# Kernel tuning notes

Hardware: AMD Instinct MI355X
Metric: run time of the kernel (lower is better)

Reference implementation:

```python
import jax, jax.numpy as jnp
import numpy as np

B, S, HID, NH = 2, 2048, 2048, 16
HD = HID // NH  # 128
BASE = 10000.0


def rope_tables(seq_len, head_dim):
    inv_freq = 1.0 / (BASE ** (jnp.arange(0, head_dim, 2, dtype=jnp.float32) / head_dim))
    t = jnp.arange(seq_len, dtype=jnp.float32)
    freqs = jnp.einsum('i,j->ij', t, inv_freq)        # [s, d/2]
    emb = jnp.concatenate([freqs, freqs], axis=-1)     # [s, d]
    return jnp.cos(emb), jnp.sin(emb)


def apply_rotary(x, cos, sin):
    # x: [b, s, h, d]; cos/sin: [s, d]
    x1, x2 = x[..., ::2], x[..., 1::2]
    c = cos[None, :, None, ::2]
    s = sin[None, :, None, ::2]
    x1r = x1 * c - x2 * s
    x2r = x1 * s + x2 * c
    return jnp.stack([x1r, x2r], axis=-1).reshape(x.shape)


def setup_inputs() -> dict:
    key = jax.random.key(0)
    ks = jax.random.split(key, 5)
    scale = 1.0 / np.sqrt(HID)
    hidden_states = jax.random.normal(ks[0], (B, S, HID), jnp.float32)
    Wq = jax.random.normal(ks[1], (HID, HID), jnp.float32) * scale
    Wk = jax.random.normal(ks[2], (HID, HID), jnp.float32) * scale
    Wv = jax.random.normal(ks[3], (HID, HID), jnp.float32) * scale
    Wo = jax.random.normal(ks[4], (HID, HID), jnp.float32) * scale
    causal = jnp.tril(jnp.ones((S, S), dtype=bool))
    attention_mask = jnp.where(causal, 0.0, -1e9).astype(jnp.float32)[None, :, :]  # [1, S, S]
    return {'hidden_states': hidden_states, 'Wq': Wq, 'Wk': Wk, 'Wv': Wv,
            'Wo': Wo, 'attention_mask': attention_mask}


def reference(hidden_states, Wq, Wk, Wv, Wo, attention_mask):
    b, s, hid = hidden_states.shape
    q = (hidden_states @ Wq.T).reshape(b, s, NH, HD)
    k = (hidden_states @ Wk.T).reshape(b, s, NH, HD)
    v = (hidden_states @ Wv.T).reshape(b, s, NH, HD)
    cos, sin = rope_tables(s, HD)
    q = apply_rotary(q, cos, sin)
    k = apply_rotary(k, cos, sin)
    # [b, h, s, d]
    q = q.transpose(0, 2, 1, 3)
    k = k.transpose(0, 2, 1, 3)
    v = v.transpose(0, 2, 1, 3)
    scores = jnp.einsum('bhqd,bhkd->bhqk', q, k) / np.sqrt(HD).astype(np.float32)
    scores = scores + attention_mask[:, None, :, :]  # broadcast mask over heads
    probs = jax.nn.softmax(scores.astype(jnp.float32), axis=-1).astype(q.dtype)
    attn = jnp.einsum('bhqk,bhkd->bhqd', probs, v)
    attn = attn.transpose(0, 2, 1, 3).reshape(b, s, hid)
    return attn @ Wo.T
```

## Files before the change

### kernel.cpp

```cpp
#include <hip/hip_runtime.h>
#include <math.h>

typedef __attribute__((ext_vector_type(8))) short short8;
typedef __attribute__((ext_vector_type(4))) float f32x4;
typedef __attribute__((ext_vector_type(16))) float f32x16;
typedef __attribute__((ext_vector_type(4))) float fvec4;
typedef __attribute__((ext_vector_type(4))) unsigned short us4;
typedef __attribute__((ext_vector_type(2))) unsigned int uint2v;

#define DI __device__ __forceinline__
#define BARX asm volatile("s_barrier" ::: "memory")
#define WAITV6 asm volatile("s_waitcnt vmcnt(6)" ::: "memory")
#define WAITV0 asm volatile("s_waitcnt vmcnt(0)" ::: "memory")
#define WAITL0 asm volatile("s_waitcnt lgkmcnt(0)" ::: "memory")
#define SCHED0 __builtin_amdgcn_sched_barrier(0)

constexpr int BB = 2, SS = 2048, HIDc = 2048, NHc = 16, HDc = 128;
constexpr int MT = BB * SS;
constexpr int KC = HIDc;

constexpr size_t OFF_HB  = 0;
constexpr size_t OFF_WB  = OFF_HB + (size_t)MT * KC * 2;
constexpr size_t OFF_Q   = OFF_WB + (size_t)4 * HIDc * KC * 2;
constexpr size_t OFF_K   = OFF_Q  + (size_t)BB * NHc * SS * HDc * 2;
constexpr size_t OFF_V   = OFF_K  + (size_t)BB * NHc * SS * HDc * 2;
constexpr size_t OFF_ATT = OFF_V  + (size_t)BB * NHc * SS * HDc * 2;
constexpr size_t OFF_COS = OFF_ATT + (size_t)MT * HIDc * 2;
constexpr size_t OFF_SIN = OFF_COS + (size_t)SS * 32 * 4;
constexpr size_t WS_NEED = OFF_SIN + (size_t)SS * 32 * 4;

DI float bf2f(unsigned short u) { union { unsigned u; float f; } v; v.u = (unsigned)u << 16; return v.f; }
DI unsigned short f2bf(float f) {
  union { float f; unsigned u; } v; v.f = f;
  unsigned r = v.u + 0x7fffu + ((v.u >> 16) & 1u);
  return (unsigned short)(r >> 16);
}

DI void gload_lds16(const void* g, void* l) {
  __builtin_amdgcn_global_load_lds((const __attribute__((address_space(1))) void*)g,
                                   (__attribute__((address_space(3))) void*)l, 16, 0, 0);
}

DI unsigned cvtpk_bf16(float lo, float hi_) {
  unsigned r;
  asm("v_cvt_pk_bf16_f32 %0, %1, %2" : "=v"(r) : "v"(lo), "v"(hi_));
  return r;
}

__global__ void __launch_bounds__(256) cvt_kernel(
    const float* __restrict__ H,  const float* __restrict__ W0,
    const float* __restrict__ W1, const float* __restrict__ W2,
    const float* __restrict__ W3, unsigned short* __restrict__ dst)
{
  constexpr size_t HN = (size_t)MT * KC;
  constexpr size_t WN = (size_t)HIDc * KC;
  size_t e0 = ((size_t)blockIdx.x * 256 + threadIdx.x) * 8;
  const float* src; size_t off;
  if (e0 < HN) { src = H; off = e0; }
  else {
    size_t t = e0 - HN; int a = (int)(t >> 22);
    src = (a == 0) ? W0 : (a == 1) ? W1 : (a == 2) ? W2 : W3;
    off = t & (WN - 1);
  }
  fvec4 v0 = *(const fvec4*)(src + off);
  fvec4 v1 = *(const fvec4*)(src + off + 4);
  short8 o;
  o[0] = (short)f2bf(v0[0]); o[1] = (short)f2bf(v0[1]);
  o[2] = (short)f2bf(v0[2]); o[3] = (short)f2bf(v0[3]);
  o[4] = (short)f2bf(v1[0]); o[5] = (short)f2bf(v1[1]);
  o[6] = (short)f2bf(v1[2]); o[7] = (short)f2bf(v1[3]);
  *(short8*)(dst + e0) = o;
}

__global__ void __launch_bounds__(256) rope_tab_kernel(float* __restrict__ cosT,
                                                       float* __restrict__ sinT)
{
  int idx = blockIdx.x * 256 + threadIdx.x;
  int t = idx >> 5, fi = idx & 31;
  float inv = powf(10000.0f, -(float)fi * (1.0f / 32.0f));
  float ang = (float)t * inv;
  cosT[idx] = cosf(ang);
  sinT[idx] = sinf(ang);
}

template<int EPI, int NBX>
__global__ void __launch_bounds__(512, 2) gemm8(
    const unsigned short* __restrict__ A,
    const unsigned short* __restrict__ Bw,
    void* __restrict__ dq, void* __restrict__ dk, void* __restrict__ dv)
{
  __shared__ __align__(16) unsigned short Al[3][256 * 64];
  __shared__ __align__(16) unsigned short Bl[3][128 * 64];
  const int tid = threadIdx.x, lane = tid & 63, w = tid >> 6;
  const int wm = w >> 1, wn = w & 1;
  const int ln15 = lane & 15, lq = lane >> 4;

  const int xcd = blockIdx.x & 7, idx = blockIdx.x >> 3;
  const int by = xcd * 2 + idx / NBX, bx = idx % NBX;
  const int m0 = by * 256, n0 = bx * 128;

  const int srow = tid >> 3;
  const int sc = (tid & 7) ^ (srow & 7);
  const unsigned short* asrc[4];
  const unsigned short* bsrc[2];
#pragma unroll
  for (int l = 0; l < 4; ++l) asrc[l] = A  + (size_t)(m0 + l * 64 + srow) * KC + sc * 8;
#pragma unroll
  for (int l = 0; l < 2; ++l) bsrc[l] = Bw + (size_t)(n0 + l * 64 + srow) * KC + sc * 8;

  const int x7 = ln15 & 7;
  const int slA0 = (lq ^ x7) * 8;
  const int slA1 = ((4 + lq) ^ x7) * 8;
  int rA[4], rB[4];
#pragma unroll
  for (int i = 0; i < 4; ++i) rA[i] = (wm * 64 + i * 16 + ln15) * 64;
#pragma unroll
  for (int j = 0; j < 4; ++j) rB[j] = (wn * 64 + j * 16 + ln15) * 64;

  constexpr int NT = KC / 64;
  auto stA = [&](int kt, int buf, int l) {
    gload_lds16(asrc[l] + (size_t)kt * 64, &Al[buf][(size_t)(l * 512 + w * 64) * 8]);
  };
  auto stB = [&](int kt, int buf, int l) {
    gload_lds16(bsrc[l] + (size_t)kt * 64, &Bl[buf][(size_t)(l * 512 + w * 64) * 8]);
  };

  stA(0, 0, 0); stA(0, 0, 1); stA(0, 0, 2); stA(0, 0, 3); stB(0, 0, 0); stB(0, 0, 1);
  stA(1, 1, 0); stA(1, 1, 1); stA(1, 1, 2); stA(1, 1, 3); stB(1, 1, 0); stB(1, 1, 1);
  WAITV6; BARX;

  f32x4 acc[4][4] = {};
  int cb = 0, nb = 2;
  for (int kt = 0; kt < NT; ++kt) {
    const unsigned short* Ac = &Al[cb][0];
    const unsigned short* Bc = &Bl[cb][0];
    const bool pf = (kt + 2 < NT);
    short8 a01[2][2], a23[2][2], bf[4][2];

#pragma unroll
    for (int i = 0; i < 2; ++i) {
      a01[i][0] = *(const short8*)&Ac[rA[i] + slA0];
      a01[i][1] = *(const short8*)&Ac[rA[i] + slA1];
    }
#pragma unroll
    for (int j = 0; j < 4; ++j) {
      bf[j][0] = *(const short8*)&Bc[rB[j] + slA0];
      bf[j][1] = *(const short8*)&Bc[rB[j] + slA1];
    }
    if (pf) { stA(kt + 2, nb, 0); stA(kt + 2, nb, 1); stA(kt + 2, nb, 2); }
    BARX;
    WAITL0; SCHED0;
    __builtin_amdgcn_s_setprio(1);
#pragma unroll
    for (int i = 0; i < 2; ++i)
#pragma unroll
      for (int j = 0; j < 4; ++j)
#pragma unroll
        for (int k = 0; k < 2; ++k)
          acc[i][j] = __builtin_amdgcn_mfma_f32_16x16x32_bf16(a01[i][k], bf[j][k], acc[i][j], 0, 0, 0);
    __builtin_amdgcn_s_setprio(0);
    BARX;

#pragma unroll
    for (int i = 0; i < 2; ++i) {
      a23[i][0] = *(const short8*)&Ac[rA[2 + i] + slA0];
      a23[i][1] = *(const short8*)&Ac[rA[2 + i] + slA1];
    }
    if (pf) { stA(kt + 2, nb, 3); stB(kt + 2, nb, 0); stB(kt + 2, nb, 1); }
    BARX;
    WAITL0; SCHED0;
    __builtin_amdgcn_s_setprio(1);
#pragma unroll
    for (int i = 0; i < 2; ++i)
#pragma unroll
      for (int j = 0; j < 4; ++j)
#pragma unroll
        for (int k = 0; k < 2; ++k)
          acc[2 + i][j] = __builtin_amdgcn_mfma_f32_16x16x32_bf16(a23[i][k], bf[j][k], acc[2 + i][j], 0, 0, 0);
    __builtin_amdgcn_s_setprio(0);
    if (kt < NT - 2) { WAITV6; }
    else if (kt == NT - 2) { WAITV0; }
    BARX;

    cb = (cb == 2) ? 0 : cb + 1;
    nb = (nb == 2) ? 0 : nb + 1;
  }

  if (EPI == 0) {
#pragma unroll
    for (int i = 0; i < 4; ++i)
#pragma unroll
      for (int j = 0; j < 4; ++j) {
        int colb = n0 + wn * 64 + j * 16;
        int z = colb >> 11;
        int c2 = (colb & 2047) + ln15;
        int h = c2 >> 7, d = c2 & 127;
        int m = m0 + wm * 64 + i * 16 + lq * 4;
        int b = m >> 11, s = m & 2047;
        if (z == 2) {
          us4 pk;
#pragma unroll
          for (int r = 0; r < 4; ++r) pk[r] = f2bf(acc[i][j][r]);
          *(us4*)((unsigned short*)dv + (((size_t)b * NHc + h) * HDc + d) * SS + s) = pk;
        } else {
          unsigned short* D = (unsigned short*)(z ? dk : dq);
#pragma unroll
          for (int r = 0; r < 4; ++r)
            D[(((size_t)b * NHc + h) * SS + s + r) * HDc + d] = f2bf(acc[i][j][r]);
        }
      }
  } else {
    float* O = (float*)dq;
#pragma unroll
    for (int i = 0; i < 4; ++i)
#pragma unroll
      for (int j = 0; j < 4; ++j) {
        int col = n0 + wn * 64 + j * 16 + ln15;
        int m = m0 + wm * 64 + i * 16 + lq * 4;
#pragma unroll
        for (int r = 0; r < 4; ++r)
          O[(size_t)(m + r) * HIDc + col] = acc[i][j][r];
      }
  }
}

__global__ void __launch_bounds__(256) rope_kernel(
    unsigned int* __restrict__ Q, unsigned int* __restrict__ Kd,
    const float* __restrict__ cosT, const float* __restrict__ sinT)
{
  constexpr size_t NP = (size_t)BB * NHc * SS * 64;
  size_t gid = (size_t)blockIdx.x * 256 + threadIdx.x;
  unsigned int* P = (gid < NP) ? Q : Kd;
  size_t r = (gid < NP) ? gid : gid - NP;
  int j  = (int)(r & 63);
  int s  = (int)((r >> 6) & (SS - 1));
  int fi = j & 31;
  float c  = cosT[s * 32 + fi];
  float sn = sinT[s * 32 + fi];
  unsigned v = P[r];
  float x1 = bf2f((unsigned short)(v & 0xffff));
  float x2 = bf2f((unsigned short)(v >> 16));
  float y1 = x1 * c - x2 * sn;
  float y2 = x1 * sn + x2 * c;
  P[r] = (unsigned)f2bf(y1) | ((unsigned)f2bf(y2) << 16);
}

__global__ void __launch_bounds__(512, 2) attn_kernel(
    const unsigned short* __restrict__ Qg,
    const unsigned short* __restrict__ Kg,
    const unsigned short* __restrict__ Vg,
    unsigned short* __restrict__ Og)
{
  __shared__ __align__(16) unsigned short Klds[2][64 * 128];
  __shared__ __align__(16) unsigned short Vlds[2][128 * 64];
  __shared__ __align__(16) unsigned short Plds[8][32 * 64];
  const int tid = threadIdx.x, lane = tid & 63, w = tid >> 6;
  const int l31 = lane & 31, hi = lane >> 5;

  const int wg = blockIdx.x;
  const int xcd = wg & 7, idx = wg >> 3;
  const int bh = xcd + 8 * (idx & 3);
  const int tt = idx >> 2;

  const int qtile = (w < 2) ? tt : (w < 4) ? (tt + 8) : (w < 6) ? (31 - tt) : (23 - tt);
  const int sub1 = w & 1;
  const int q0w = qtile * 64 + sub1 * 32;
  const int ntiles = 32 - tt;

  const size_t hbase = (size_t)bh * SS * HDc;
  const float CE = 1.44269504089f * 0.08838834764831845f;
  const int b = bh >> 4, h = bh & 15;

  short8 qf[8];
#pragma unroll
  for (int ks = 0; ks < 8; ++ks)
    qf[ks] = *(const short8*)(Qg + hbase + (size_t)(q0w + l31) * HDc + ks * 16 + hi * 8);

  f32x16 accO[4];
#pragma unroll
  for (int db = 0; db < 4; ++db)
#pragma unroll
    for (int r = 0; r < 16; ++r) accO[db][r] = 0.f;
  float mr = -1e30f, lr = 0.f;

  auto stage = [&](int kvt, int buf) {
    const int kv0 = kvt * 64;
#pragma unroll
    for (int p = 0; p < 2; ++p) {
      int c = p * 512 + tid;
      int krow = c >> 4, ksl = c & 15;
      gload_lds16(Kg + hbase + (size_t)(kv0 + krow) * HDc + ((ksl ^ (krow & 7)) << 3),
                  (unsigned short*)&Klds[buf][0] + (size_t)c * 8);
      int vd = c >> 3, vsl = c & 7;
      gload_lds16(Vg + hbase + (size_t)vd * SS + kv0 + ((vsl ^ (vd & 7)) << 3),
                  (unsigned short*)&Vlds[buf][0] + (size_t)c * 8);
    }
  };

  stage(0, 0);
  __syncthreads();
  int cur = 0;
  for (int kvt = 0; kvt < ntiles; ++kvt) {
    if (kvt + 1 < ntiles) stage(kvt + 1, cur ^ 1);

    if (kvt <= qtile) {
      const bool diag = (kvt == qtile);
      const bool haveT1 = (!diag) || sub1;

      f32x16 s0, s1;
#pragma unroll
      for (int r = 0; r < 16; ++r) s0[r] = 0.f;
      __builtin_amdgcn_s_setprio(1);
#pragma unroll
      for (int ks = 0; ks < 8; ++ks) {
        int row = l31;
        short8 kf = *(const short8*)&Klds[cur][row * 128 + (((2 * ks + hi) ^ (row & 7)) << 3)];
        s0 = __builtin_amdgcn_mfma_f32_32x32x16_bf16(kf, qf[ks], s0, 0, 0, 0);
      }
      if (haveT1) {
#pragma unroll
        for (int r = 0; r < 16; ++r) s1[r] = 0.f;
#pragma unroll
        for (int ks = 0; ks < 8; ++ks) {
          int row = 32 + l31;
          short8 kf = *(const short8*)&Klds[cur][row * 128 + (((2 * ks + hi) ^ (row & 7)) << 3)];
          s1 = __builtin_amdgcn_mfma_f32_32x32x16_bf16(kf, qf[ks], s1, 0, 0, 0);
        }
      }
      __builtin_amdgcn_s_setprio(0);

      if (diag) {
        if (sub1) {
#pragma unroll
          for (int r = 0; r < 16; ++r)
            if (((r & 3) + 8 * (r >> 2) + 4 * hi) > l31) s1[r] = -1e30f;
        } else {
#pragma unroll
          for (int r = 0; r < 16; ++r)
            if (((r & 3) + 8 * (r >> 2) + 4 * hi) > l31) s0[r] = -1e30f;
        }
      }

      float pmax = s0[0];
#pragma unroll
      for (int r = 1; r < 16; ++r) pmax = fmaxf(pmax, s0[r]);
      if (haveT1) {
#pragma unroll
        for (int r = 0; r < 16; ++r) pmax = fmaxf(pmax, s1[r]);
      }
      pmax = fmaxf(pmax, __shfl_xor(pmax, 32));

      int grow = (CE * (pmax - mr) > 8.0f) ? 1 : 0;
      if (__any(grow)) {
        float mn = fmaxf(mr, pmax);
        float al = exp2f(CE * (mr - mn));
        mr = mn; lr *= al;
        float alr[16];
#pragma unroll
        for (int r = 0; r < 16; ++r)
          alr[r] = __shfl(al, (r & 3) + 8 * (r >> 2) + 4 * hi);
#pragma unroll
        for (int db = 0; db < 4; ++db)
#pragma unroll
          for (int r = 0; r < 16; ++r) accO[db][r] *= alr[r];
      }

      float psum = 0.f;
#pragma unroll
      for (int r = 0; r < 16; ++r) {
        float p = exp2f(CE * (s0[r] - mr));
        s0[r] = p; psum += p;
      }
      if (haveT1) {
#pragma unroll
        for (int r = 0; r < 16; ++r) {
          float p = exp2f(CE * (s1[r] - mr));
          s1[r] = p; psum += p;
        }
      }
      psum += __shfl_xor(psum, 32);
      lr += psum;

#pragma unroll
      for (int i = 0; i < 4; ++i) {
        uint2v pk;
        pk[0] = cvtpk_bf16(s0[4 * i], s0[4 * i + 1]);
        pk[1] = cvtpk_bf16(s0[4 * i + 2], s0[4 * i + 3]);
        int chunk = i ^ (l31 & 7);
        *(uint2v*)&Plds[w][l31 * 64 + chunk * 8 + hi * 4] = pk;
      }
      if (haveT1) {
#pragma unroll
        for (int i = 0; i < 4; ++i) {
          uint2v pk;
          pk[0] = cvtpk_bf16(s1[4 * i], s1[4 * i + 1]);
          pk[1] = cvtpk_bf16(s1[4 * i + 2], s1[4 * i + 3]);
          int chunk = (4 + i) ^ (l31 & 7);
          *(uint2v*)&Plds[w][l31 * 64 + chunk * 8 + hi * 4] = pk;
        }
      }

      short8 ap[4];
#pragma unroll
      for (int ks = 0; ks < 2; ++ks)
        ap[ks] = *(const short8*)&Plds[w][l31 * 64 + (((2 * ks + hi) ^ (l31 & 7)) << 3)];
      if (haveT1) {
#pragma unroll
        for (int ks = 2; ks < 4; ++ks)
          ap[ks] = *(const short8*)&Plds[w][l31 * 64 + (((2 * ks + hi) ^ (l31 & 7)) << 3)];
      }

      __builtin_amdgcn_s_setprio(1);
#pragma unroll
      for (int db = 0; db < 4; ++db) {
        int row = db * 32 + l31;
#pragma unroll
        for (int ks = 0; ks < 2; ++ks) {
          short8 vf = *(const short8*)&Vlds[cur][row * 64 + (((2 * ks + hi) ^ (row & 7)) << 3)];
          accO[db] = __builtin_amdgcn_mfma_f32_32x32x16_bf16(ap[ks], vf, accO[db], 0, 0, 0);
        }
      }
      if (haveT1) {
#pragma unroll
        for (int db = 0; db < 4; ++db) {
          int row = db * 32 + l31;
#pragma unroll
          for (int ks = 2; ks < 4; ++ks) {
            short8 vf = *(const short8*)&Vlds[cur][row * 64 + (((2 * ks + hi) ^ (row & 7)) << 3)];
            accO[db] = __builtin_amdgcn_mfma_f32_32x32x16_bf16(ap[ks], vf, accO[db], 0, 0, 0);
          }
        }
      }
      __builtin_amdgcn_s_setprio(0);
    }

    __syncthreads();
    cur ^= 1;
  }

  float il = 1.0f / lr;
  float ilr[16];
#pragma unroll
  for (int r = 0; r < 16; ++r)
    ilr[r] = __shfl(il, (r & 3) + 8 * (r >> 2) + 4 * hi);
#pragma unroll
  for (int db = 0; db < 4; ++db)
#pragma unroll
    for (int r = 0; r < 16; ++r) {
      int q = q0w + (r & 3) + 8 * (r >> 2) + 4 * hi;
      int d = db * 32 + l31;
      Og[((size_t)b * SS + q) * HIDc + h * HDc + d] = f2bf(accO[db][r] * ilr[r]);
    }
}

extern "C" void kernel_launch(void* const* d_in, const int* in_sizes, int n_in,
                              void* d_out, int out_size, void* d_ws, size_t ws_size,
                              hipStream_t stream)
{
  if (ws_size < WS_NEED) return;

  const float* H  = (const float*)d_in[0];
  const float* Wq = (const float*)d_in[1];
  const float* Wk = (const float*)d_in[2];
  const float* Wv = (const float*)d_in[3];
  const float* Wo = (const float*)d_in[4];
  char* ws = (char*)d_ws;
  unsigned short* HB = (unsigned short*)(ws + OFF_HB);
  unsigned short* WB = (unsigned short*)(ws + OFF_WB);
  unsigned short* Qb = (unsigned short*)(ws + OFF_Q);
  unsigned short* Kb = (unsigned short*)(ws + OFF_K);
  unsigned short* Vb = (unsigned short*)(ws + OFF_V);
  unsigned short* AT = (unsigned short*)(ws + OFF_ATT);
  float* cosT = (float*)(ws + OFF_COS);
  float* sinT = (float*)(ws + OFF_SIN);

  cvt_kernel<<<12288, 256, 0, stream>>>(H, Wq, Wk, Wv, Wo, HB);
  rope_tab_kernel<<<256, 256, 0, stream>>>(cosT, sinT);
  gemm8<0, 48><<<768, 512, 0, stream>>>(HB, WB, Qb, Kb, Vb);
  rope_kernel<<<32768, 256, 0, stream>>>((unsigned*)Qb, (unsigned*)Kb, cosT, sinT);
  attn_kernel<<<256, 512, 0, stream>>>(Qb, Kb, Vb, AT);
  gemm8<1, 16><<<256, 512, 0, stream>>>(AT, WB + (size_t)3 * HIDc * KC,
                                        d_out, nullptr, nullptr);
}
```

Measured before the change: 273.5 us.

## Add 256x256-tile QKV GEMM kernel with 4-stage K=32 pipeline

```diff
diff --git a/kernel.cpp b/kernel.cpp
--- a/kernel.cpp
+++ b/kernel.cpp
@@ -10,7 +10,9 @@
 
 #define DI __device__ __forceinline__
 #define BARX asm volatile("s_barrier" ::: "memory")
+#define WAITV8 asm volatile("s_waitcnt vmcnt(8)" ::: "memory")
 #define WAITV6 asm volatile("s_waitcnt vmcnt(6)" ::: "memory")
+#define WAITV4 asm volatile("s_waitcnt vmcnt(4)" ::: "memory")
 #define WAITV0 asm volatile("s_waitcnt vmcnt(0)" ::: "memory")
 #define WAITL0 asm volatile("s_waitcnt lgkmcnt(0)" ::: "memory")
 #define SCHED0 __builtin_amdgcn_sched_barrier(0)
@@ -83,6 +85,118 @@
   sinT[idx] = sinf(ang);
 }
 
+template<int NBX>
+__global__ void __launch_bounds__(512, 2) gemmQKV(
+    const unsigned short* __restrict__ A,
+    const unsigned short* __restrict__ Bw,
+    void* __restrict__ dq, void* __restrict__ dk, void* __restrict__ dv)
+{
+  __shared__ __align__(16) unsigned short Al[4][256 * 32];
+  __shared__ __align__(16) unsigned short Bl[4][256 * 32];
+  const int tid = threadIdx.x, lane = tid & 63, w = tid >> 6;
+  const int wm = w >> 2, wn = w & 3;
+  const int ln15 = lane & 15, lq = lane >> 4;
+
+  const int xcd = blockIdx.x & 7, idx = blockIdx.x >> 3;
+  const int by = xcd * 2 + idx / NBX, bx = idx % NBX;
+  const int m0 = by * 256, n0 = bx * 256;
+
+  const unsigned short* asrc[2];
+  const unsigned short* bsrc[2];
+#pragma unroll
+  for (int l = 0; l < 2; ++l) {
+    int c = l * 512 + tid;
+    int row = c >> 2, sp = c & 3;
+    int sc = sp ^ (row & 3);
+    asrc[l] = A  + (size_t)(m0 + row) * KC + sc * 8;
+    bsrc[l] = Bw + (size_t)(n0 + row) * KC + sc * 8;
+  }
+
+  const int slA = (lq ^ (ln15 & 3)) * 8;
+  int rA[8], rB[4];
+#pragma unroll
+  for (int i = 0; i < 8; ++i) rA[i] = (wm * 128 + i * 16 + ln15) * 32;
+#pragma unroll
+  for (int j = 0; j < 4; ++j) rB[j] = (wn * 64 + j * 16 + ln15) * 32;
+
+  constexpr int NT = KC / 32;
+  auto stA = [&](int kt, int l) {
+    gload_lds16(asrc[l] + (size_t)kt * 32, &Al[kt & 3][(size_t)(l * 512 + w * 64) * 8]);
+  };
+  auto stB = [&](int kt, int l) {
+    gload_lds16(bsrc[l] + (size_t)kt * 32, &Bl[kt & 3][(size_t)(l * 512 + w * 64) * 8]);
+  };
+
+  stA(0, 0); stA(0, 1); stB(0, 0); stB(0, 1);
+  stA(1, 0); stA(1, 1); stB(1, 0); stB(1, 1);
+  stA(2, 0); stA(2, 1); stB(2, 0); stB(2, 1);
+  WAITV8; BARX;
+
+  f32x4 acc[8][4] = {};
+  for (int kt = 0; kt < NT; ++kt) {
+    const unsigned short* Ac = &Al[kt & 3][0];
+    const unsigned short* Bc = &Bl[kt & 3][0];
+    const bool pf = (kt + 3 < NT);
+    short8 af[4], bfr[4];
+
+#pragma unroll
+    for (int j = 0; j < 4; ++j) bfr[j] = *(const short8*)&Bc[rB[j] + slA];
+#pragma unroll
+    for (int i = 0; i < 4; ++i) af[i] = *(const short8*)&Ac[rA[i] + slA];
+    if (pf) { stA(kt + 3, 0); stA(kt + 3, 1); }
+    BARX;
+    WAITL0; SCHED0;
+    __builtin_amdgcn_s_setprio(1);
+#pragma unroll
+    for (int i = 0; i < 4; ++i)
+#pragma unroll
+      for (int j = 0; j < 4; ++j)
+        acc[i][j] = __builtin_amdgcn_mfma_f32_16x16x32_bf16(af[i], bfr[j], acc[i][j], 0, 0, 0);
+    __builtin_amdgcn_s_setprio(0);
+    BARX;
+
+#pragma unroll
+    for (int i = 0; i < 4; ++i) af[i] = *(const short8*)&Ac[rA[4 + i] + slA];
+    if (pf) { stB(kt + 3, 0); stB(kt + 3, 1); }
+    BARX;
+    WAITL0; SCHED0;
+    __builtin_amdgcn_s_setprio(1);
+#pragma unroll
+    for (int i = 0; i < 4; ++i)
+#pragma unroll
+      for (int j = 0; j < 4; ++j)
+        acc[4 + i][j] = __builtin_amdgcn_mfma_f32_16x16x32_bf16(af[i], bfr[j], acc[4 + i][j], 0, 0, 0);
+    __builtin_amdgcn_s_setprio(0);
+    if (kt < NT - 3) { WAITV8; }
+    else if (kt == NT - 3) { WAITV4; }
+    else if (kt == NT - 2) { WAITV0; }
+    BARX;
+  }
+
+#pragma unroll
+  for (int i = 0; i < 8; ++i)
+#pragma unroll
+    for (int j = 0; j < 4; ++j) {
+      int col = n0 + wn * 64 + j * 16 + ln15;
+      int z = col >> 11;
+      int c2 = col & 2047;
+      int h = c2 >> 7, d = c2 & 127;
+      int m = m0 + wm * 128 + i * 16 + lq * 4;
+      int b = m >> 11, s = m & 2047;
+      if (z == 2) {
+        us4 pk;
+#pragma unroll
+        for (int r = 0; r < 4; ++r) pk[r] = f2bf(acc[i][j][r]);
+        *(us4*)((unsigned short*)dv + (((size_t)b * NHc + h) * HDc + d) * SS + s) = pk;
+      } else {
+        unsigned short* D = (unsigned short*)(z ? dk : dq);
+#pragma unroll
+        for (int r = 0; r < 4; ++r)
+          D[(((size_t)b * NHc + h) * SS + s + r) * HDc + d] = f2bf(acc[i][j][r]);
+      }
+    }
+}
+
 template<int EPI, int NBX>
 __global__ void __launch_bounds__(512, 2) gemm8(
     const unsigned short* __restrict__ A,
@@ -476,7 +590,7 @@
 
   cvt_kernel<<<12288, 256, 0, stream>>>(H, Wq, Wk, Wv, Wo, HB);
   rope_tab_kernel<<<256, 256, 0, stream>>>(cosT, sinT);
-  gemm8<0, 48><<<768, 512, 0, stream>>>(HB, WB, Qb, Kb, Vb);
+  gemmQKV<24><<<384, 512, 0, stream>>>(HB, WB, Qb, Kb, Vb);
   rope_kernel<<<32768, 256, 0, stream>>>((unsigned*)Qb, (unsigned*)Kb, cosT, sinT);
   attn_kernel<<<256, 512, 0, stream>>>(Qb, Kb, Vb, AT);
   gemm8<1, 16><<<256, 512, 0, stream>>>(AT, WB + (size_t)3 * HIDc * KC,
```

Result: slower. 292.4 us (+6.9%).
